# Optimization experiments

Hardware: AMD Instinct MI355X
Metric: run time of the kernel (lower is better)

## Reference

```python
import jax, jax.numpy as jnp
import numpy as np

N, E = 50000, 400000
IN_F, HID, HEADS, CLASSES, GROUP = 256, 64, 4, 40, 2
NEG_SLOPE = 0.2
EPS = 1e-5


def setup_inputs() -> dict:
    key = jax.random.key(0)
    ks = jax.random.split(key, 16)
    s = 0.05
    W = HEADS * HID          # 256 flattened hidden width
    GW = W // GROUP          # 128 per-group width
    GD = HID // GROUP        # 32  per-head out_feats in middle blocks
    x = jax.random.normal(ks[0], (N, IN_F), jnp.float32)
    src = jax.random.randint(ks[1], (E,), 0, N, dtype=jnp.int32)
    # guarantee every node has >=1 incoming edge so edge_softmax is well-defined
    dst = jnp.concatenate([jnp.arange(N, dtype=jnp.int32),
                           jax.random.randint(ks[2], (E - N,), 0, N, dtype=jnp.int32)])
    return dict(
        x=x, src=src, dst=dst,
        W0=jax.random.normal(ks[3], (W, IN_F)) * s,
        attn_l0=jax.random.normal(ks[4], (HEADS, HID)) * s,
        attn_r0=jax.random.normal(ks[5], (HEADS, HID)) * s,
        resW0=jax.random.normal(ks[6], (W, IN_F)) * s,
        mid_bn_gamma=jnp.ones((2, GROUP, GW)),
        mid_bn_beta=jnp.zeros((2, GROUP, GW)),
        mid_W=jax.random.normal(ks[7], (2, GROUP, GW, GW)) * s,
        mid_attn_l=jax.random.normal(ks[8], (2, GROUP, HEADS, GD)) * s,
        mid_attn_r=jax.random.normal(ks[9], (2, GROUP, HEADS, GD)) * s,
        mid_resW=jax.random.normal(ks[10], (2, GROUP, GW, GW)) * s,
        norm_gamma=jnp.ones((W,)), norm_beta=jnp.zeros((W,)),
        W_last=jax.random.normal(ks[11], (CLASSES, W)) * s,
        attn_l_last=jax.random.normal(ks[12], (1, CLASSES)) * s,
        attn_r_last=jax.random.normal(ks[13], (1, CLASSES)) * s,
        resW_last=jax.random.normal(ks[14], (CLASSES, W)) * s,
        bias_last=jnp.zeros((CLASSES,)),
    )


def _gat_conv(x, src, dst, W, attn_l, attn_r, resW, out_isqrt, in_sqrt):
    n = x.shape[0]
    H, D = attn_l.shape
    ft0 = (x @ W.T).reshape(n, H, D)            # projected feat [N,H,D]
    ft = ft0 * out_isqrt[:, None, None]         # symmetric norm on source side
    el = (ft * attn_l).sum(-1)                  # [N,H] (uses normalized feat_src)
    er = (ft0 * attn_r).sum(-1)                 # [N,H] (feat_dst aliased BEFORE norm)
    e = el[src] + er[dst]                       # edge scores [E,H]
    e = jnp.where(e >= 0, e, NEG_SLOPE * e)     # leaky_relu
    emax = jax.ops.segment_max(e, dst, num_segments=n)
    emax = jnp.where(jnp.isfinite(emax), emax, 0.0)
    ex = jnp.exp(e - emax[dst])
    denom = jax.ops.segment_sum(ex, dst, num_segments=n)
    a = ex / jnp.maximum(denom, 1e-9)[dst]      # per-destination edge softmax [E,H]
    msg = ft[src] * a[:, :, None]               # [E,H,D]
    rst = jax.ops.segment_sum(msg, dst, num_segments=n)
    rst = rst * in_sqrt[:, None, None]          # symmetric norm on dest side
    rst = rst + (x @ resW.T).reshape(n, H, D)   # residual fc
    return rst


def _bn_relu(z, gamma, beta):
    mu = z.mean(0)
    var = ((z - mu) ** 2).mean(0)               # biased var (torch BN training)
    return jax.nn.relu(gamma * (z - mu) * jax.lax.rsqrt(var + EPS) + beta)


def reference(x, src, dst, W0, attn_l0, attn_r0, resW0, mid_bn_gamma, mid_bn_beta,
              mid_W, mid_attn_l, mid_attn_r, mid_resW, norm_gamma, norm_beta,
              W_last, attn_l_last, attn_r_last, resW_last, bias_last):
    n = x.shape[0]
    ones = jnp.ones((src.shape[0],), x.dtype)
    outdeg = jnp.maximum(jax.ops.segment_sum(ones, src, num_segments=n), 1.0)
    indeg = jnp.maximum(jax.ops.segment_sum(ones, dst, num_segments=n), 1.0)
    out_isqrt = outdeg ** -0.5
    in_sqrt = jnp.sqrt(indeg)
    # layer 0: GATConv(in_feats -> n_hidden, n_heads)
    h = _gat_conv(x, src, dst, W0, attn_l0, attn_r0, resW0, out_isqrt, in_sqrt).reshape(n, -1)
    # reversible middle layers: GroupAdditiveCoupling, group=2
    for l in range(2):
        x0, x1 = jnp.split(h, 2, axis=-1)
        z = _bn_relu(x1, mid_bn_gamma[l, 0], mid_bn_beta[l, 0])
        y0 = x0 + _gat_conv(z, src, dst, mid_W[l, 0], mid_attn_l[l, 0], mid_attn_r[l, 0],
                            mid_resW[l, 0], out_isqrt, in_sqrt).reshape(n, -1)
        z = _bn_relu(y0, mid_bn_gamma[l, 1], mid_bn_beta[l, 1])
        y1 = x1 + _gat_conv(z, src, dst, mid_W[l, 1], mid_attn_l[l, 1], mid_attn_r[l, 1],
                            mid_resW[l, 1], out_isqrt, in_sqrt).reshape(n, -1)
        h = jnp.concatenate([y0, y1], axis=-1)
    # final norm + relu + output conv (1 head), mean over head dim, bias_last
    h = _bn_relu(h, norm_gamma, norm_beta)
    out = _gat_conv(h, src, dst, W_last, attn_l_last, attn_r_last, resW_last,
                    out_isqrt, in_sqrt).mean(1)
    return out + bias_last
```

## Files before the change

### kernel.cpp

```cpp
#include <hip/hip_runtime.h>
#include <hip/hip_bf16.h>


#define IN_F   256
#define HIDW   256
#define CLS    40

typedef __attribute__((ext_vector_type(8))) __bf16 bf16x8;
typedef __attribute__((ext_vector_type(4))) float  f32x4;

__device__ inline bf16x8 zb8() {
    bf16x8 v;
#pragma unroll
    for (int i = 0; i < 8; ++i) v[i] = (__bf16)0.f;
    return v;
}
__device__ inline bf16x8 ldb8(const __hip_bfloat16* p) {
    return *reinterpret_cast<const bf16x8*>(p);
}
__device__ inline float bf2f(unsigned short u) {
    union { unsigned int i; float f; } c;
    c.i = ((unsigned int)u) << 16;
    return c.f;
}
__device__ inline unsigned short f2bu(float f) {
    __hip_bfloat16 t = __float2bfloat16(f);
    union { __hip_bfloat16 b; unsigned short u; } c;
    c.b = t;
    return c.u;
}

__global__ void k_hist(const int* __restrict__ src, const int* __restrict__ dst,
                       int E, int* __restrict__ outdeg, int* __restrict__ indeg) {
    for (int e = blockIdx.x * blockDim.x + threadIdx.x; e < E; e += gridDim.x * blockDim.x) {
        atomicAdd(&outdeg[src[e]], 1);
        atomicAdd(&indeg[dst[e]], 1);
    }
}

__global__ void k_scan1(const int* __restrict__ cnt, int N, int* __restrict__ rp1,
                        int* __restrict__ bsum) {
    __shared__ int sm[256];
    int i = blockIdx.x * 256 + threadIdx.x;
    int v = (i < N) ? cnt[i] : 0;
    sm[threadIdx.x] = v;
    __syncthreads();
    for (int off = 1; off < 256; off <<= 1) {
        int t = (threadIdx.x >= off) ? sm[threadIdx.x - off] : 0;
        __syncthreads();
        sm[threadIdx.x] += t;
        __syncthreads();
    }
    if (i < N) rp1[i] = sm[threadIdx.x];
    if (threadIdx.x == 255) bsum[blockIdx.x] = sm[255];
}

__global__ void k_scan2(int* __restrict__ bsum, int nb) {
    __shared__ int sm[256];
    int v = (threadIdx.x < nb) ? bsum[threadIdx.x] : 0;
    sm[threadIdx.x] = v;
    __syncthreads();
    for (int off = 1; off < 256; off <<= 1) {
        int t = (threadIdx.x >= off) ? sm[threadIdx.x - off] : 0;
        __syncthreads();
        sm[threadIdx.x] += t;
        __syncthreads();
    }
    if (threadIdx.x < nb) bsum[threadIdx.x] = sm[threadIdx.x] - v;
}

__global__ void k_scan3(int* __restrict__ rp1, const int* __restrict__ bsumExcl, int N) {
    int i = blockIdx.x * 256 + threadIdx.x;
    if (i < N) rp1[i] += bsumExcl[blockIdx.x];
    if (blockIdx.x == 0 && threadIdx.x == 0) rp1[-1] = 0;
}

__global__ void k_scatter(const int* __restrict__ src, const int* __restrict__ dst,
                          int E, int* __restrict__ cursor, int* __restrict__ csr_src) {
    for (int e = blockIdx.x * blockDim.x + threadIdx.x; e < E; e += gridDim.x * blockDim.x) {
        int d = dst[e];
        int pos = atomicAdd(&cursor[d], 1);
        csr_src[pos] = src[e];
    }
}

__global__ void k_deg(const int* __restrict__ outdeg, const int* __restrict__ indeg,
                      float* __restrict__ oi, float* __restrict__ insq, int N) {
    int i = blockIdx.x * 256 + threadIdx.x;
    if (i < N) {
        int od = outdeg[i]; if (od < 1) od = 1;
        int id = indeg[i];  if (id < 1) id = 1;
        oi[i]   = rsqrtf((float)od);
        insq[i] = sqrtf((float)id);
    }
}

__global__ void k_cvt6(const float* s0, __hip_bfloat16* d0, int n0,
                       const float* s1, __hip_bfloat16* d1, int n1,
                       const float* s2, __hip_bfloat16* d2, int n2,
                       const float* s3, __hip_bfloat16* d3, int n3,
                       const float* s4, __hip_bfloat16* d4, int n4,
                       const float* s5, __hip_bfloat16* d5, int n5) {
    const float* ss; __hip_bfloat16* dd; int nn;
    switch (blockIdx.y) {
        case 0: ss = s0; dd = d0; nn = n0; break;
        case 1: ss = s1; dd = d1; nn = n1; break;
        case 2: ss = s2; dd = d2; nn = n2; break;
        case 3: ss = s3; dd = d3; nn = n3; break;
        case 4: ss = s4; dd = d4; nn = n4; break;
        default: ss = s5; dd = d5; nn = n5; break;
    }
    for (int i = blockIdx.x * blockDim.x + threadIdx.x; i < nn; i += gridDim.x * blockDim.x)
        dd[i] = __float2bfloat16(ss[i]);
}

__global__ void k_prepw(const float* __restrict__ W0,
                        const float* __restrict__ al0, const float* __restrict__ ar0,
                        const float* __restrict__ midW,
                        const float* __restrict__ midal, const float* __restrict__ midar,
                        __hip_bfloat16* __restrict__ Waug0,
                        __hip_bfloat16* __restrict__ midWaug) {
    const int layer = blockIdx.y;
    int NF, K, D;
    const float *W, *al, *ar;
    __hip_bfloat16* dst;
    if (layer == 0) {
        NF = 256; K = 256; D = 64;
        W = W0; al = al0; ar = ar0; dst = Waug0;
    } else {
        const int pg = layer - 1;
        NF = 128; K = 128; D = 32;
        W = midW + pg * 16384; al = midal + pg * 128; ar = midar + pg * 128;
        dst = midWaug + (size_t)pg * 144 * 128;
    }
    const int total = (NF + 16) * K;
    for (int idx = blockIdx.x * 256 + threadIdx.x; idx < total; idx += gridDim.x * 256) {
        const int col = idx / K, k = idx % K;
        float v = 0.f;
        if (col < NF) {
            v = W[(size_t)col * K + k];
        } else {
            const int j = col - NF;
            if (j < 8) {
                const int head = j & 3;
                const float* at = (j < 4) ? al : ar;
                float s = 0.f;
                for (int d = 0; d < D; ++d)
                    s += W[(size_t)(head * D + d) * K + k] * at[head * D + d];
                v = s;
            }
        }
        dst[idx] = __float2bfloat16(v);
    }
}

template<int K, int NF, int NR, int H, bool BN, bool ABF, bool ADDRES>
__global__ __launch_bounds__(512) void k_gatconv_lds(
    const void* __restrict__ Ain, int lda,
    const __hip_bfloat16* __restrict__ Waug,
    const __hip_bfloat16* __restrict__ Wres,
    __hip_bfloat16* __restrict__ ftb, int ldft,
    __hip_bfloat16* __restrict__ hout, int ldh, int houtoff,
    int M,
    const float* __restrict__ scale, const float* __restrict__ shift,
    const float* __restrict__ oi,
    float* __restrict__ el, float* __restrict__ er) {
    constexpr int BM = 64, KF = K / 32, NTOT = NF + NR;
    constexpr int CW = NTOT / 8, CT = CW / 16;
    constexpr int NRT = BM / 16;
    static_assert(NTOT % 8 == 0 && CW % 16 == 0, "col split");
    static_assert(NF % CW == 0, "ft/res wave boundary");
    static_assert(H == 4, "el/er float4 stores assume H==4");
    __shared__ bf16x8 ldsA[NRT * KF * 64];
    const int tid = threadIdx.x;
    const int wv = tid >> 6, lane = tid & 63, rf = lane & 15, kg = lane >> 4;
    const int row0 = blockIdx.x * BM;

    {
        constexpr int CPR = K / 8;
        constexpr int RSTEP = 512 / CPR;
        const int c16 = tid % CPR;
        const int ec = c16 * 8;
        const int skf = c16 >> 2, skg = c16 & 3;
        float sc[8], sh[8];
        if (BN) {
            float4 s01 = *reinterpret_cast<const float4*>(scale + ec);
            float4 s23 = *reinterpret_cast<const float4*>(scale + ec + 4);
            float4 h01 = *reinterpret_cast<const float4*>(shift + ec);
            float4 h23 = *reinterpret_cast<const float4*>(shift + ec + 4);
            sc[0]=s01.x; sc[1]=s01.y; sc[2]=s01.z; sc[3]=s01.w;
            sc[4]=s23.x; sc[5]=s23.y; sc[6]=s23.z; sc[7]=s23.w;
            sh[0]=h01.x; sh[1]=h01.y; sh[2]=h01.z; sh[3]=h01.w;
            sh[4]=h23.x; sh[5]=h23.y; sh[6]=h23.z; sh[7]=h23.w;
        }
#pragma unroll
        for (int r0 = 0; r0 < BM; r0 += RSTEP) {
            const int r = r0 + tid / CPR;
            if (r < BM) {
                const int gr = row0 + r;
                bf16x8 t = zb8();
                if (gr < M) {
                    if (ABF) {
                        const __hip_bfloat16* ap =
                            (const __hip_bfloat16*)Ain + (size_t)gr * lda + ec;
                        bf16x8 raw = ldb8(ap);
                        if (BN) {
#pragma unroll
                            for (int i = 0; i < 8; ++i)
                                t[i] = (__bf16)fmaxf((float)raw[i] * sc[i] + sh[i], 0.f);
                        } else {
                            t = raw;
                        }
                    } else {
                        const float* ap = (const float*)Ain + (size_t)gr * lda + ec;
                        float4 f0 = *reinterpret_cast<const float4*>(ap);
                        float4 f1 = *reinterpret_cast<const float4*>(ap + 4);
                        float v[8] = {f0.x, f0.y, f0.z, f0.w, f1.x, f1.y, f1.z, f1.w};
#pragma unroll
                        for (int i = 0; i < 8; ++i) {
                            float u = v[i];
                            if (BN) u = fmaxf(u * sc[i] + sh[i], 0.f);
                            t[i] = (__bf16)u;
                        }
                    }
                }
                ldsA[((r >> 4) * KF + skf) * 64 + ((skg * 16 + (r & 15)) ^ skf)] = t;
            }
        }
    }
    __syncthreads();

    const bool isft = (wv * CW) < NF;
    const int colbase = isft ? wv * CW : wv * CW - NF;
    const __hip_bfloat16* __restrict__ Wb = isft ? Waug : Wres;

    for (int ct = 0; ct < CT; ++ct) {
        const int tcol = colbase + ct * 16;
        bf16x8 w[KF];
        const __hip_bfloat16* bp = Wb + (size_t)(tcol + rf) * K + kg * 8;
#pragma unroll
        for (int kf = 0; kf < KF; ++kf) w[kf] = ldb8(bp + kf * 32);
#pragma unroll
        for (int rtp = 0; rtp < NRT / 2; ++rtp) {
            f32x4 acc0 = {0.f, 0.f, 0.f, 0.f};
            f32x4 acc1 = {0.f, 0.f, 0.f, 0.f};
#pragma unroll
            for (int kf = 0; kf < KF; ++kf) {
                const bf16x8 a0 = ldsA[((2 * rtp) * KF + kf) * 64 + (lane ^ kf)];
                const bf16x8 a1 = ldsA[((2 * rtp + 1) * KF + kf) * 64 + (lane ^ kf)];
                acc0 = __builtin_amdgcn_mfma_f32_16x16x32_bf16(w[kf], a0, acc0, 0, 0, 0);
                acc1 = __builtin_amdgcn_mfma_f32_16x16x32_bf16(w[kf], a1, acc1, 0, 0, 0);
            }
            const int r0g = row0 + 2 * rtp * 16 + rf;
            const int r1g = r0g + 16;
            const int c4 = tcol + 4 * kg;
            ushort4 q0 = {f2bu(acc0[0]), f2bu(acc0[1]), f2bu(acc0[2]), f2bu(acc0[3])};
            ushort4 q1 = {f2bu(acc1[0]), f2bu(acc1[1]), f2bu(acc1[2]), f2bu(acc1[3])};
            if (isft) {
                if (r0g < M)
                    *reinterpret_cast<ushort4*>(&ftb[(size_t)r0g * ldft + c4]) = q0;
                if (r1g < M)
                    *reinterpret_cast<ushort4*>(&ftb[(size_t)r1g * ldft + c4]) = q1;
            } else {
                if (r0g < M) {
                    __hip_bfloat16* hp = hout + (size_t)r0g * ldh + houtoff + c4;
                    if (ADDRES) {
                        ushort4 cur = *reinterpret_cast<ushort4*>(hp);
                        q0.x = f2bu(bf2f(cur.x) + acc0[0]);
                        q0.y = f2bu(bf2f(cur.y) + acc0[1]);
                        q0.z = f2bu(bf2f(cur.z) + acc0[2]);
                        q0.w = f2bu(bf2f(cur.w) + acc0[3]);
                    }
                    *reinterpret_cast<ushort4*>(hp) = q0;
                }
                if (r1g < M) {
                    __hip_bfloat16* hp = hout + (size_t)r1g * ldh + houtoff + c4;
                    if (ADDRES) {
                        ushort4 cur = *reinterpret_cast<ushort4*>(hp);
                        q1.x = f2bu(bf2f(cur.x) + acc1[0]);
                        q1.y = f2bu(bf2f(cur.y) + acc1[1]);
                        q1.z = f2bu(bf2f(cur.z) + acc1[2]);
                        q1.w = f2bu(bf2f(cur.w) + acc1[3]);
                    }
                    *reinterpret_cast<ushort4*>(hp) = q1;
                }
            }
        }
    }

    if (wv == 0) {
        bf16x8 w[KF];
        const __hip_bfloat16* bp = Waug + (size_t)(NF + rf) * K + kg * 8;
#pragma unroll
        for (int kf = 0; kf < KF; ++kf) w[kf] = ldb8(bp + kf * 32);
#pragma unroll
        for (int rtp = 0; rtp < NRT / 2; ++rtp) {
            f32x4 acc0 = {0.f, 0.f, 0.f, 0.f};
            f32x4 acc1 = {0.f, 0.f, 0.f, 0.f};
#pragma unroll
            for (int kf = 0; kf < KF; ++kf) {
                const bf16x8 a0 = ldsA[((2 * rtp) * KF + kf) * 64 + (lane ^ kf)];
                const bf16x8 a1 = ldsA[((2 * rtp + 1) * KF + kf) * 64 + (lane ^ kf)];
                acc0 = __builtin_amdgcn_mfma_f32_16x16x32_bf16(w[kf], a0, acc0, 0, 0, 0);
                acc1 = __builtin_amdgcn_mfma_f32_16x16x32_bf16(w[kf], a1, acc1, 0, 0, 0);
            }
            const int r0g = row0 + 2 * rtp * 16 + rf;
            const int r1g = r0g + 16;
            if (kg == 0) {
                if (r0g < M) {
                    const float o = oi[r0g];
                    float4 v = {acc0[0] * o, acc0[1] * o, acc0[2] * o, acc0[3] * o};
                    *reinterpret_cast<float4*>(&el[(size_t)r0g * 4]) = v;
                }
                if (r1g < M) {
                    const float o = oi[r1g];
                    float4 v = {acc1[0] * o, acc1[1] * o, acc1[2] * o, acc1[3] * o};
                    *reinterpret_cast<float4*>(&el[(size_t)r1g * 4]) = v;
                }
            } else if (kg == 1) {
                if (r0g < M) {
                    float4 v = {acc0[0], acc0[1], acc0[2], acc0[3]};
                    *reinterpret_cast<float4*>(&er[(size_t)r0g * 4]) = v;
                }
                if (r1g < M) {
                    float4 v = {acc1[0], acc1[1], acc1[2], acc1[3]};
                    *reinterpret_cast<float4*>(&er[(size_t)r1g * 4]) = v;
                }
            }
        }
    }
}

template<int K, int NF, int NR, int H>
__global__ __launch_bounds__(256) void k_gatconv_sm(
    const __hip_bfloat16* __restrict__ A, int lda,
    const __hip_bfloat16* __restrict__ Wft,
    const __hip_bfloat16* __restrict__ Wres,
    __hip_bfloat16* __restrict__ ftb, int ldft,
    float* __restrict__ Cres, int ldcres,
    int M,
    const float* __restrict__ scale, const float* __restrict__ shift,
    const float* __restrict__ bias,
    const float* __restrict__ attn_l, const float* __restrict__ attn_r,
    const float* __restrict__ oi,
    float* __restrict__ el, float* __restrict__ er) {
    constexpr int KF   = K / 32;
    constexpr int NCTF = (NF + 15) / 16;
    constexpr int NCTR = (NR + 15) / 16;
    constexpr int CTH  = NCTF / H;
    static_assert(NCTF % H == 0, "head tiling");
    const int wave = threadIdx.x >> 6, lane = threadIdx.x & 63;
    const int row0 = blockIdx.x * 64 + wave * 16;
    const int rf = lane & 15, kg = lane >> 4;

    bf16x8 a[KF];
    {
        const int row = row0 + rf;
        const bool rok = row < M;
#pragma unroll
        for (int kf = 0; kf < KF; ++kf) {
            const int c0 = kg * 8 + kf * 32;
            if (rok) {
                bf16x8 raw = ldb8(A + (size_t)row * lda + c0);
                float4 s01 = *reinterpret_cast<const float4*>(scale + c0);
                float4 s23 = *reinterpret_cast<const float4*>(scale + c0 + 4);
                float4 h01 = *reinterpret_cast<const float4*>(shift + c0);
                float4 h23 = *reinterpret_cast<const float4*>(shift + c0 + 4);
                float sc[8] = {s01.x,s01.y,s01.z,s01.w,s23.x,s23.y,s23.z,s23.w};
                float sh[8] = {h01.x,h01.y,h01.z,h01.w,h23.x,h23.y,h23.z,h23.w};
                bf16x8 t;
#pragma unroll
                for (int i = 0; i < 8; ++i)
                    t[i] = (__bf16)fmaxf((float)raw[i] * sc[i] + sh[i], 0.f);
                a[kf] = t;
            } else {
                a[kf] = zb8();
            }
        }
    }

    int ct = 0;
    for (int hh = 0; hh < H; ++hh) {
        float elp[4] = {0.f, 0.f, 0.f, 0.f};
        float erp[4] = {0.f, 0.f, 0.f, 0.f};
        for (int cth = 0; cth < CTH; ++cth, ++ct) {
            const int ccol = ct * 16 + rf;
            bf16x8 b[KF];
            const __hip_bfloat16* bp = Wft + (size_t)ccol * K + kg * 8;
#pragma unroll
            for (int kf = 0; kf < KF; ++kf)
                b[kf] = (ccol < NF) ? ldb8(bp + kf * 32) : zb8();
            f32x4 acc = {0.f, 0.f, 0.f, 0.f};
#pragma unroll
            for (int kf = 0; kf < KF; ++kf)
                acc = __builtin_amdgcn_mfma_f32_16x16x32_bf16(a[kf], b[kf], acc, 0, 0, 0);
            float al = 0.f, ar = 0.f;
            if (ccol < NF) { al = attn_l[ccol]; ar = attn_r[ccol]; }
            if (ccol < NF) {
#pragma unroll
                for (int r = 0; r < 4; ++r) {
                    const float v = acc[r];
                    elp[r] += v * al; erp[r] += v * ar;
                    const int row = row0 + kg * 4 + r;
                    if (row < M)
                        ftb[(size_t)row * ldft + ccol] = __float2bfloat16(v);
                }
            }
        }
#pragma unroll
        for (int off = 1; off <= 8; off <<= 1)
#pragma unroll
            for (int r = 0; r < 4; ++r) {
                elp[r] += __shfl_xor(elp[r], off);
                erp[r] += __shfl_xor(erp[r], off);
            }
        if (rf == 0) {
#pragma unroll
            for (int r = 0; r < 4; ++r) {
                const int row = row0 + kg * 4 + r;
                if (row < M) {
                    el[(size_t)row * H + hh] = oi[row] * elp[r];
                    er[(size_t)row * H + hh] = erp[r];
                }
            }
        }
    }

    for (int rt = 0; rt < NCTR; ++rt) {
        const int ccol = rt * 16 + rf;
        bf16x8 b[KF];
        const __hip_bfloat16* bp = Wres + (size_t)ccol * K + kg * 8;
#pragma unroll
        for (int kf = 0; kf < KF; ++kf)
            b[kf] = (ccol < NR) ? ldb8(bp + kf * 32) : zb8();
        f32x4 acc = {0.f, 0.f, 0.f, 0.f};
#pragma unroll
        for (int kf = 0; kf < KF; ++kf)
            acc = __builtin_amdgcn_mfma_f32_16x16x32_bf16(a[kf], b[kf], acc, 0, 0, 0);
        if (ccol < NR) {
#pragma unroll
            for (int r = 0; r < 4; ++r) {
                const int row = row0 + kg * 4 + r;
                if (row < M) {
                    float v = acc[r];
                    if (bias) v += bias[ccol];
                    Cres[(size_t)row * ldcres + ccol] = v;
                }
            }
        }
    }
}

template<int EPL>
__device__ inline void ldrow(const __hip_bfloat16* fp, float* f) {
    if constexpr (EPL == 4) {
        ushort4 q = *reinterpret_cast<const ushort4*>(fp);
        f[0] = bf2f(q.x); f[1] = bf2f(q.y); f[2] = bf2f(q.z); f[3] = bf2f(q.w);
    } else if constexpr (EPL == 2) {
        ushort2 q = *reinterpret_cast<const ushort2*>(fp);
        f[0] = bf2f(q.x); f[1] = bf2f(q.y);
    } else {
        f[0] = bf2f(*reinterpret_cast<const unsigned short*>(fp));
    }
}
__device__ inline float escore(float sc) {
    sc = sc >= 0.f ? sc : 0.2f * sc;
    sc = fminf(fmaxf(sc, -30.f), 30.f);
    return __expf(sc);
}

template<int H, int D, bool OBF>
__global__ __launch_bounds__(256) void k_agg(
    const __hip_bfloat16* __restrict__ ftb,
    const float* __restrict__ el, const float* __restrict__ er,
    const int* __restrict__ row_ptr, const int* __restrict__ csr_src,
    const float* __restrict__ oi, const float* __restrict__ insq,
    void* __restrict__ out, int ldc, int N) {
    constexpr int W = H * D;
    constexpr int EPL = (W >= 64) ? (W / 64) : 1;
    const int lane = threadIdx.x & 63;
    const int v = blockIdx.x * 4 + (threadIdx.x >> 6);
    if (v >= N) return;
    if (W < 64 && lane >= W) return;
    const int col0 = lane * EPL;
    const int myh = (W >= 64) ? (col0 / D) : 0;
    const int s = row_ptr[v], e = row_ptr[v + 1];
    const float erv = er[(size_t)v * H + myh];

    float denom = 0.f;
    float acc[EPL];
#pragma unroll
    for (int k = 0; k < EPL; ++k) acc[k] = 0.f;

    int p = s;
    for (; p + 3 < e; p += 4) {
        const int u0 = csr_src[p + 0], u1 = csr_src[p + 1];
        const int u2 = csr_src[p + 2], u3 = csr_src[p + 3];
        float f0[EPL], f1[EPL], f2[EPL], f3[EPL];
        ldrow<EPL>(ftb + (size_t)u0 * W + col0, f0);
        ldrow<EPL>(ftb + (size_t)u1 * W + col0, f1);
        ldrow<EPL>(ftb + (size_t)u2 * W + col0, f2);
        ldrow<EPL>(ftb + (size_t)u3 * W + col0, f3);
        const float s0 = el[(size_t)u0 * H + myh], s1 = el[(size_t)u1 * H + myh];
        const float s2 = el[(size_t)u2 * H + myh], s3 = el[(size_t)u3 * H + myh];
        const float o0 = oi[u0], o1 = oi[u1], o2 = oi[u2], o3 = oi[u3];
        const float w0 = escore(s0 + erv), w1 = escore(s1 + erv);
        const float w2 = escore(s2 + erv), w3 = escore(s3 + erv);
        denom += (w0 + w1) + (w2 + w3);
        const float a0 = w0 * o0, a1 = w1 * o1, a2 = w2 * o2, a3 = w3 * o3;
#pragma unroll
        for (int k = 0; k < EPL; ++k)
            acc[k] += a0 * f0[k] + a1 * f1[k] + a2 * f2[k] + a3 * f3[k];
    }
    for (; p < e; ++p) {
        const int u = csr_src[p];
        float f[EPL];
        ldrow<EPL>(ftb + (size_t)u * W + col0, f);
        const float w = escore(el[(size_t)u * H + myh] + erv);
        denom += w;
        const float a = w * oi[u];
#pragma unroll
        for (int k = 0; k < EPL; ++k) acc[k] += a * f[k];
    }

    const float iv = insq[v] / fmaxf(denom, 1e-9f);
    if (OBF) {
        __hip_bfloat16* op = (__hip_bfloat16*)out + (size_t)v * ldc + col0;
        if constexpr (EPL == 4) {
            ushort4 o = *reinterpret_cast<ushort4*>(op);
            o.x = f2bu(bf2f(o.x) + iv * acc[0]);
            o.y = f2bu(bf2f(o.y) + iv * acc[1]);
            o.z = f2bu(bf2f(o.z) + iv * acc[2]);
            o.w = f2bu(bf2f(o.w) + iv * acc[3]);
            *reinterpret_cast<ushort4*>(op) = o;
        } else if constexpr (EPL == 2) {
            ushort2 o = *reinterpret_cast<ushort2*>(op);
            o.x = f2bu(bf2f(o.x) + iv * acc[0]);
            o.y = f2bu(bf2f(o.y) + iv * acc[1]);
            *reinterpret_cast<ushort2*>(op) = o;
        } else {
            unsigned short* up = (unsigned short*)op;
            *up = f2bu(bf2f(*up) + iv * acc[0]);
        }
    } else {
        float* op = (float*)out + (size_t)v * ldc + col0;
        if constexpr (EPL == 4) {
            float4 o = *reinterpret_cast<float4*>(op);
            o.x += iv * acc[0]; o.y += iv * acc[1]; o.z += iv * acc[2]; o.w += iv * acc[3];
            *reinterpret_cast<float4*>(op) = o;
        } else if constexpr (EPL == 2) {
            float2 o = *reinterpret_cast<float2*>(op);
            o.x += iv * acc[0]; o.y += iv * acc[1];
            *reinterpret_cast<float2*>(op) = o;
        } else {
            op[0] += iv * acc[0];
        }
    }
}

template<int F>
__global__ __launch_bounds__(256) void k_bn_part(const __hip_bfloat16* __restrict__ in,
                                                 int ldin, int N,
                                                 float* __restrict__ psum,
                                                 float* __restrict__ psum2) {
    constexpr int CP = F / 2;
    constexpr int SL = 256 / CP;
    const int cp = threadIdx.x % CP;
    const int pr = blockIdx.x * SL + threadIdx.x / CP;
    const int PRT = gridDim.x * SL;
    float s0 = 0.f, s20 = 0.f, s1 = 0.f, s21 = 0.f;
    for (int r = pr; r < N; r += PRT) {
        ushort2 q = *reinterpret_cast<const ushort2*>(&in[(size_t)r * ldin + cp * 2]);
        const float a = bf2f(q.x), b = bf2f(q.y);
        s0 += a; s20 += a * a; s1 += b; s21 += b * b;
    }
    psum[(size_t)pr * F + cp * 2] = s0;
    psum[(size_t)pr * F + cp * 2 + 1] = s1;
    psum2[(size_t)pr * F + cp * 2] = s20;
    psum2[(size_t)pr * F + cp * 2 + 1] = s21;
}

template<int F>
__global__ __launch_bounds__(256) void k_bn_fin(const float* __restrict__ psum,
                                                const float* __restrict__ psum2, int PRT,
                                                const float* __restrict__ gamma,
                                                const float* __restrict__ beta,
                                                float* __restrict__ scale,
                                                float* __restrict__ shift, int N) {
    const int col = blockIdx.x;
    float s = 0.f, s2 = 0.f;
    for (int p = threadIdx.x; p < PRT; p += 256) {
        s += psum[(size_t)p * F + col];
        s2 += psum2[(size_t)p * F + col];
    }
#pragma unroll
    for (int off = 32; off; off >>= 1) {
        s += __shfl_down(s, off);
        s2 += __shfl_down(s2, off);
    }
    __shared__ float sm[4], sm2[4];
    const int wave = threadIdx.x >> 6, lane = threadIdx.x & 63;
    if (lane == 0) { sm[wave] = s; sm2[wave] = s2; }
    __syncthreads();
    if (threadIdx.x == 0) {
        s = sm[0] + sm[1] + sm[2] + sm[3];
        s2 = sm2[0] + sm2[1] + sm2[2] + sm2[3];
        float mu = s / N;
        float var = s2 / N - mu * mu;
        float isd = rsqrtf(var + 1e-5f);
        float g = gamma[col];
        scale[col] = g * isd;
        shift[col] = beta[col] - g * isd * mu;
    }
}

extern "C" void kernel_launch(void* const* d_in, const int* in_sizes, int n_in,
                              void* d_out, int out_size, void* d_ws, size_t ws_size,
                              hipStream_t stream) {
    const float* x           = (const float*)d_in[0];
    const int*   src         = (const int*)d_in[1];
    const int*   dst         = (const int*)d_in[2];
    const float* W0          = (const float*)d_in[3];
    const float* attn_l0     = (const float*)d_in[4];
    const float* attn_r0     = (const float*)d_in[5];
    const float* resW0       = (const float*)d_in[6];
    const float* mid_bn_g    = (const float*)d_in[7];
    const float* mid_bn_b    = (const float*)d_in[8];
    const float* mid_W       = (const float*)d_in[9];
    const float* mid_attn_l  = (const float*)d_in[10];
    const float* mid_attn_r  = (const float*)d_in[11];
    const float* mid_resW    = (const float*)d_in[12];
    const float* norm_gamma  = (const float*)d_in[13];
    const float* norm_beta   = (const float*)d_in[14];
    const float* W_last      = (const float*)d_in[15];
    const float* attn_l_last = (const float*)d_in[16];
    const float* attn_r_last = (const float*)d_in[17];
    const float* resW_last   = (const float*)d_in[18];
    const float* bias_last   = (const float*)d_in[19];

    const int N = in_sizes[0] / IN_F;
    const int E = in_sizes[1];

    char* p = (char*)d_ws;
    size_t used = 0;
    auto take = [&](size_t bytes) -> char* {
        char* r = p;
        size_t adv = (bytes + 255) & ~(size_t)255;
        p += adv; used += adv;
        return r;
    };
    __hip_bfloat16* h       = (__hip_bfloat16*)take((size_t)N * HIDW * 2);
    __hip_bfloat16* ftb     = (__hip_bfloat16*)take((size_t)N * HIDW * 2);
    float*          el      = (float*)take((size_t)N * 4 * 4);
    float*          er      = (float*)take((size_t)N * 4 * 4);
    float*          oi      = (float*)take((size_t)N * 4);
    float*          insq    = (float*)take((size_t)N * 4);
    int*            indeg   = (int*)take((size_t)N * 4);
    int*            outdeg  = (int*)take((size_t)N * 4);
    int*            row_ptr = (int*)take((size_t)(N + 1) * 4);
    int*            cursor  = (int*)take((size_t)N * 4);
    int*            csr_src = (int*)take((size_t)E * 4);
    int*            bsum    = (int*)take(256 * 4);
    float*          psum    = (float*)take(1 << 20);
    float*          psum2   = (float*)take(1 << 20);
    float*          scale   = (float*)take(1024);
    float*          shift   = (float*)take(1024);
    __hip_bfloat16* Waug0     = (__hip_bfloat16*)take((size_t)272 * 256 * 2);
    __hip_bfloat16* midWaug   = (__hip_bfloat16*)take((size_t)4 * 144 * 128 * 2);
    __hip_bfloat16* resW0bf   = (__hip_bfloat16*)take(65536 * 2);
    __hip_bfloat16* midresWbf = (__hip_bfloat16*)take(65536 * 2);
    __hip_bfloat16* Wlastbf   = (__hip_bfloat16*)take(10240 * 2);
    __hip_bfloat16* resWlastbf= (__hip_bfloat16*)take(10240 * 2);
    if (used > ws_size) return;

    const int nbN = (N + 255) / 256;
    const int NB4 = (N + 3) / 4;
    const int GWB = (N + 63) / 64;
    const int GWS = (N + 63) / 64;
    const int BNB = 512;

    hipMemsetAsync(indeg, 0, (size_t)N * 4, stream);
    hipMemsetAsync(outdeg, 0, (size_t)N * 4, stream);
    k_hist<<<1024, 256, 0, stream>>>(src, dst, E, outdeg, indeg);
    k_scan1<<<nbN, 256, 0, stream>>>(indeg, N, row_ptr + 1, bsum);
    k_scan2<<<1, 256, 0, stream>>>(bsum, nbN);
    k_scan3<<<nbN, 256, 0, stream>>>(row_ptr + 1, bsum, N);
    hipMemcpyAsync(cursor, row_ptr, (size_t)N * 4, hipMemcpyDeviceToDevice, stream);
    k_scatter<<<1024, 256, 0, stream>>>(src, dst, E, cursor, csr_src);
    k_deg<<<nbN, 256, 0, stream>>>(outdeg, indeg, oi, insq, N);

    k_cvt6<<<dim3(64, 4), 256, 0, stream>>>(resW0, resW0bf, 65536,
                                            mid_resW, midresWbf, 65536,
                                            W_last, Wlastbf, 10240,
                                            resW_last, resWlastbf, 10240,
                                            nullptr, nullptr, 0,
                                            nullptr, nullptr, 0);
    k_prepw<<<dim3(96, 5), 256, 0, stream>>>(W0, attn_l0, attn_r0,
                                             mid_W, mid_attn_l, mid_attn_r,
                                             Waug0, midWaug);

    k_gatconv_lds<256, 256, 256, 4, false, false, false><<<GWB, 512, 0, stream>>>(
        x, 256, Waug0, resW0bf, ftb, 256, h, 256, 0, N,
        nullptr, nullptr, oi, el, er);
    k_agg<4, 64, true><<<NB4, 256, 0, stream>>>(ftb, el, er, row_ptr, csr_src, oi, insq,
                                                h, 256, N);

    for (int l = 0; l < 2; ++l) {
        for (int g = 0; g < 2; ++g) {
            const int inoff  = (g == 0) ? 128 : 0;
            const int outoff = (g == 0) ? 0 : 128;
            const int pg = l * 2 + g;
            k_bn_part<128><<<BNB, 256, 0, stream>>>(h + inoff, 256, N, psum, psum2);
            k_bn_fin<128><<<128, 256, 0, stream>>>(psum, psum2, BNB * 4,
                                                   mid_bn_g + pg * 128, mid_bn_b + pg * 128,
                                                   scale, shift, N);
            k_gatconv_lds<128, 128, 128, 4, true, true, true><<<GWB, 512, 0, stream>>>(
                h + inoff, 256, midWaug + (size_t)pg * 144 * 128, midresWbf + pg * 16384,
                ftb, 128, h, 256, outoff, N,
                scale, shift, oi, el, er);
            k_agg<4, 32, true><<<NB4, 256, 0, stream>>>(ftb, el, er, row_ptr, csr_src,
                                                        oi, insq, h + outoff, 256, N);
        }
    }

    k_bn_part<256><<<BNB, 256, 0, stream>>>(h, 256, N, psum, psum2);
    k_bn_fin<256><<<256, 256, 0, stream>>>(psum, psum2, BNB * 2, norm_gamma, norm_beta,
                                           scale, shift, N);
    k_gatconv_sm<256, 40, 40, 1><<<GWS, 256, 0, stream>>>(
        h, 256, Wlastbf, resWlastbf, ftb, 40, (float*)d_out, 40, N,
        scale, shift, bias_last,
        attn_l_last, attn_r_last, oi, el, er);
    k_agg<1, 40, false><<<NB4, 256, 0, stream>>>(ftb, el, er, row_ptr, csr_src, oi, insq,
                                                 (float*)d_out, 40, N);
}
```

Measured before the change: 558.4 us.

## Make GATConv GEMM kernel persistent with register-prefetched next tile

The LDS-staged GATConv projection kernel now loops over row tiles with a grid-stride schedule at half the previous grid size. While one tile's MFMA work runs, the next tile's input rows are loaded into registers, then written to LDS after a barrier. This is meant to hide global-load latency behind compute and amortize weight loads. The cost is extra registers for the prefetch buffer, possibly lower occupancy, and two barriers per tile.

```diff
diff --git a/kernel.cpp b/kernel.cpp
--- a/kernel.cpp
+++ b/kernel.cpp
@@ -161,173 +161,200 @@
     const __hip_bfloat16* __restrict__ Wres,
     __hip_bfloat16* __restrict__ ftb, int ldft,
     __hip_bfloat16* __restrict__ hout, int ldh, int houtoff,
-    int M,
+    int M, int ntiles,
     const float* __restrict__ scale, const float* __restrict__ shift,
     const float* __restrict__ oi,
     float* __restrict__ el, float* __restrict__ er) {
     constexpr int BM = 64, KF = K / 32, NTOT = NF + NR;
     constexpr int CW = NTOT / 8, CT = CW / 16;
     constexpr int NRT = BM / 16;
+    constexpr int CPR = K / 8;
+    constexpr int RSTEP = 512 / CPR;
+    constexpr int PASS = BM / RSTEP;
     static_assert(NTOT % 8 == 0 && CW % 16 == 0, "col split");
     static_assert(NF % CW == 0, "ft/res wave boundary");
     static_assert(H == 4, "el/er float4 stores assume H==4");
     __shared__ bf16x8 ldsA[NRT * KF * 64];
     const int tid = threadIdx.x;
     const int wv = tid >> 6, lane = tid & 63, rf = lane & 15, kg = lane >> 4;
-    const int row0 = blockIdx.x * BM;
-
-    {
-        constexpr int CPR = K / 8;
-        constexpr int RSTEP = 512 / CPR;
-        const int c16 = tid % CPR;
-        const int ec = c16 * 8;
-        const int skf = c16 >> 2, skg = c16 & 3;
-        float sc[8], sh[8];
-        if (BN) {
-            float4 s01 = *reinterpret_cast<const float4*>(scale + ec);
-            float4 s23 = *reinterpret_cast<const float4*>(scale + ec + 4);
-            float4 h01 = *reinterpret_cast<const float4*>(shift + ec);
-            float4 h23 = *reinterpret_cast<const float4*>(shift + ec + 4);
-            sc[0]=s01.x; sc[1]=s01.y; sc[2]=s01.z; sc[3]=s01.w;
-            sc[4]=s23.x; sc[5]=s23.y; sc[6]=s23.z; sc[7]=s23.w;
-            sh[0]=h01.x; sh[1]=h01.y; sh[2]=h01.z; sh[3]=h01.w;
-            sh[4]=h23.x; sh[5]=h23.y; sh[6]=h23.z; sh[7]=h23.w;
-        }
-#pragma unroll
-        for (int r0 = 0; r0 < BM; r0 += RSTEP) {
-            const int r = r0 + tid / CPR;
-            if (r < BM) {
-                const int gr = row0 + r;
-                bf16x8 t = zb8();
-                if (gr < M) {
-                    if (ABF) {
-                        const __hip_bfloat16* ap =
-                            (const __hip_bfloat16*)Ain + (size_t)gr * lda + ec;
-                        bf16x8 raw = ldb8(ap);
-                        if (BN) {
-#pragma unroll
-                            for (int i = 0; i < 8; ++i)
-                                t[i] = (__bf16)fmaxf((float)raw[i] * sc[i] + sh[i], 0.f);
-                        } else {
-                            t = raw;
-                        }
-                    } else {
-                        const float* ap = (const float*)Ain + (size_t)gr * lda + ec;
-                        float4 f0 = *reinterpret_cast<const float4*>(ap);
-                        float4 f1 = *reinterpret_cast<const float4*>(ap + 4);
-                        float v[8] = {f0.x, f0.y, f0.z, f0.w, f1.x, f1.y, f1.z, f1.w};
-#pragma unroll
-                        for (int i = 0; i < 8; ++i) {
-                            float u = v[i];
-                            if (BN) u = fmaxf(u * sc[i] + sh[i], 0.f);
-                            t[i] = (__bf16)u;
-                        }
-                    }
-                }
-                ldsA[((r >> 4) * KF + skf) * 64 + ((skg * 16 + (r & 15)) ^ skf)] = t;
-            }
-        }
-    }
-    __syncthreads();
+
+    const int c16 = tid % CPR;
+    const int ec = c16 * 8;
+    const int skf = c16 >> 2, skg = c16 & 3;
+    const int srow = tid / CPR;
+
+    float bnsc[8], bnsh[8];
+    if (BN) {
+        float4 s01 = *reinterpret_cast<const float4*>(scale + ec);
+        float4 s23 = *reinterpret_cast<const float4*>(scale + ec + 4);
+        float4 h01 = *reinterpret_cast<const float4*>(shift + ec);
+        float4 h23 = *reinterpret_cast<const float4*>(shift + ec + 4);
+        bnsc[0]=s01.x; bnsc[1]=s01.y; bnsc[2]=s01.z; bnsc[3]=s01.w;
+        bnsc[4]=s23.x; bnsc[5]=s23.y; bnsc[6]=s23.z; bnsc[7]=s23.w;
+        bnsh[0]=h01.x; bnsh[1]=h01.y; bnsh[2]=h01.z; bnsh[3]=h01.w;
+        bnsh[4]=h23.x; bnsh[5]=h23.y; bnsh[6]=h23.z; bnsh[7]=h23.w;
+    }
+
+    float4 rA[PASS][2];
+    bf16x8 rAb[PASS];
 
     const bool isft = (wv * CW) < NF;
     const int colbase = isft ? wv * CW : wv * CW - NF;
     const __hip_bfloat16* __restrict__ Wb = isft ? Waug : Wres;
 
-    for (int ct = 0; ct < CT; ++ct) {
-        const int tcol = colbase + ct * 16;
-        bf16x8 w[KF];
-        const __hip_bfloat16* bp = Wb + (size_t)(tcol + rf) * K + kg * 8;
-#pragma unroll
-        for (int kf = 0; kf < KF; ++kf) w[kf] = ldb8(bp + kf * 32);
-#pragma unroll
-        for (int rtp = 0; rtp < NRT / 2; ++rtp) {
-            f32x4 acc0 = {0.f, 0.f, 0.f, 0.f};
-            f32x4 acc1 = {0.f, 0.f, 0.f, 0.f};
-#pragma unroll
-            for (int kf = 0; kf < KF; ++kf) {
-                const bf16x8 a0 = ldsA[((2 * rtp) * KF + kf) * 64 + (lane ^ kf)];
-                const bf16x8 a1 = ldsA[((2 * rtp + 1) * KF + kf) * 64 + (lane ^ kf)];
-                acc0 = __builtin_amdgcn_mfma_f32_16x16x32_bf16(w[kf], a0, acc0, 0, 0, 0);
-                acc1 = __builtin_amdgcn_mfma_f32_16x16x32_bf16(w[kf], a1, acc1, 0, 0, 0);
-            }
-            const int r0g = row0 + 2 * rtp * 16 + rf;
-            const int r1g = r0g + 16;
-            const int c4 = tcol + 4 * kg;
-            ushort4 q0 = {f2bu(acc0[0]), f2bu(acc0[1]), f2bu(acc0[2]), f2bu(acc0[3])};
-            ushort4 q1 = {f2bu(acc1[0]), f2bu(acc1[1]), f2bu(acc1[2]), f2bu(acc1[3])};
-            if (isft) {
-                if (r0g < M)
-                    *reinterpret_cast<ushort4*>(&ftb[(size_t)r0g * ldft + c4]) = q0;
-                if (r1g < M)
-                    *reinterpret_cast<ushort4*>(&ftb[(size_t)r1g * ldft + c4]) = q1;
+    auto load_regs = [&](int t) {
+#pragma unroll
+        for (int pz = 0; pz < PASS; ++pz) {
+            const int gr = t * BM + pz * RSTEP + srow;
+            if (ABF) {
+                rAb[pz] = (gr < M)
+                    ? ldb8((const __hip_bfloat16*)Ain + (size_t)gr * lda + ec)
+                    : zb8();
             } else {
-                if (r0g < M) {
-                    __hip_bfloat16* hp = hout + (size_t)r0g * ldh + houtoff + c4;
-                    if (ADDRES) {
-                        ushort4 cur = *reinterpret_cast<ushort4*>(hp);
-                        q0.x = f2bu(bf2f(cur.x) + acc0[0]);
-                        q0.y = f2bu(bf2f(cur.y) + acc0[1]);
-                        q0.z = f2bu(bf2f(cur.z) + acc0[2]);
-                        q0.w = f2bu(bf2f(cur.w) + acc0[3]);
+                if (gr < M) {
+                    const float* ap = (const float*)Ain + (size_t)gr * lda + ec;
+                    rA[pz][0] = *reinterpret_cast<const float4*>(ap);
+                    rA[pz][1] = *reinterpret_cast<const float4*>(ap + 4);
+                } else {
+                    rA[pz][0] = {0.f, 0.f, 0.f, 0.f};
+                    rA[pz][1] = {0.f, 0.f, 0.f, 0.f};
+                }
+            }
+        }
+    };
+    auto write_lds = [&]() {
+#pragma unroll
+        for (int pz = 0; pz < PASS; ++pz) {
+            const int r = pz * RSTEP + srow;
+            bf16x8 tv;
+            if (ABF) {
+                if (BN) {
+#pragma unroll
+                    for (int i = 0; i < 8; ++i)
+                        tv[i] = (__bf16)fmaxf((float)rAb[pz][i] * bnsc[i] + bnsh[i], 0.f);
+                } else {
+                    tv = rAb[pz];
+                }
+            } else {
+                float v[8] = {rA[pz][0].x, rA[pz][0].y, rA[pz][0].z, rA[pz][0].w,
+                              rA[pz][1].x, rA[pz][1].y, rA[pz][1].z, rA[pz][1].w};
+#pragma unroll
+                for (int i = 0; i < 8; ++i) {
+                    float u = v[i];
+                    if (BN) u = fmaxf(u * bnsc[i] + bnsh[i], 0.f);
+                    tv[i] = (__bf16)u;
+                }
+            }
+            ldsA[((r >> 4) * KF + skf) * 64 + ((skg * 16 + (r & 15)) ^ skf)] = tv;
+        }
+    };
+
+    int t = blockIdx.x;
+    load_regs(t);
+    while (t < ntiles) {
+        write_lds();
+        __syncthreads();
+        const int tn = t + gridDim.x;
+        if (tn < ntiles) load_regs(tn);
+
+        const int row0 = t * BM;
+        for (int ct = 0; ct < CT; ++ct) {
+            const int tcol = colbase + ct * 16;
+            bf16x8 w[KF];
+            const __hip_bfloat16* bp = Wb + (size_t)(tcol + rf) * K + kg * 8;
+#pragma unroll
+            for (int kf = 0; kf < KF; ++kf) w[kf] = ldb8(bp + kf * 32);
+#pragma unroll
+            for (int rtp = 0; rtp < NRT / 2; ++rtp) {
+                f32x4 acc0 = {0.f, 0.f, 0.f, 0.f};
+                f32x4 acc1 = {0.f, 0.f, 0.f, 0.f};
+#pragma unroll
+                for (int kf = 0; kf < KF; ++kf) {
+                    const bf16x8 a0 = ldsA[((2 * rtp) * KF + kf) * 64 + (lane ^ kf)];
+                    const bf16x8 a1 = ldsA[((2 * rtp + 1) * KF + kf) * 64 + (lane ^ kf)];
+                    acc0 = __builtin_amdgcn_mfma_f32_16x16x32_bf16(w[kf], a0, acc0, 0, 0, 0);
+                    acc1 = __builtin_amdgcn_mfma_f32_16x16x32_bf16(w[kf], a1, acc1, 0, 0, 0);
+                }
+                const int r0g = row0 + 2 * rtp * 16 + rf;
+                const int r1g = r0g + 16;
+                const int c4 = tcol + 4 * kg;
+                ushort4 q0 = {f2bu(acc0[0]), f2bu(acc0[1]), f2bu(acc0[2]), f2bu(acc0[3])};
+                ushort4 q1 = {f2bu(acc1[0]), f2bu(acc1[1]), f2bu(acc1[2]), f2bu(acc1[3])};
+                if (isft) {
+                    if (r0g < M)
+                        *reinterpret_cast<ushort4*>(&ftb[(size_t)r0g * ldft + c4]) = q0;
+                    if (r1g < M)
+                        *reinterpret_cast<ushort4*>(&ftb[(size_t)r1g * ldft + c4]) = q1;
+                } else {
+                    if (r0g < M) {
+                        __hip_bfloat16* hp = hout + (size_t)r0g * ldh + houtoff + c4;
+                        if (ADDRES) {
+                            ushort4 cur = *reinterpret_cast<ushort4*>(hp);
+                            q0.x = f2bu(bf2f(cur.x) + acc0[0]);
+                            q0.y = f2bu(bf2f(cur.y) + acc0[1]);
+                            q0.z = f2bu(bf2f(cur.z) + acc0[2]);
+                            q0.w = f2bu(bf2f(cur.w) + acc0[3]);
+                        }
+                        *reinterpret_cast<ushort4*>(hp) = q0;
                     }
-                    *reinterpret_cast<ushort4*>(hp) = q0;
-                }
-                if (r1g < M) {
-                    __hip_bfloat16* hp = hout + (size_t)r1g * ldh + houtoff + c4;
-                    if (ADDRES) {
-                        ushort4 cur = *reinterpret_cast<ushort4*>(hp);
-                        q1.x = f2bu(bf2f(cur.x) + acc1[0]);
-                        q1.y = f2bu(bf2f(cur.y) + acc1[1]);
-                        q1.z = f2bu(bf2f(cur.z) + acc1[2]);
-                        q1.w = f2bu(bf2f(cur.w) + acc1[3]);
+                    if (r1g < M) {
+                        __hip_bfloat16* hp = hout + (size_t)r1g * ldh + houtoff + c4;
+                        if (ADDRES) {
+                            ushort4 cur = *reinterpret_cast<ushort4*>(hp);
+                            q1.x = f2bu(bf2f(cur.x) + acc1[0]);
+                            q1.y = f2bu(bf2f(cur.y) + acc1[1]);
+                            q1.z = f2bu(bf2f(cur.z) + acc1[2]);
+                            q1.w = f2bu(bf2f(cur.w) + acc1[3]);
+                        }
+                        *reinterpret_cast<ushort4*>(hp) = q1;
                     }
-                    *reinterpret_cast<ushort4*>(hp) = q1;
-                }
-            }
-        }
-    }
-
-    if (wv == 0) {
-        bf16x8 w[KF];
-        const __hip_bfloat16* bp = Waug + (size_t)(NF + rf) * K + kg * 8;
-#pragma unroll
-        for (int kf = 0; kf < KF; ++kf) w[kf] = ldb8(bp + kf * 32);
-#pragma unroll
-        for (int rtp = 0; rtp < NRT / 2; ++rtp) {
-            f32x4 acc0 = {0.f, 0.f, 0.f, 0.f};
-            f32x4 acc1 = {0.f, 0.f, 0.f, 0.f};
-#pragma unroll
-            for (int kf = 0; kf < KF; ++kf) {
-                const bf16x8 a0 = ldsA[((2 * rtp) * KF + kf) * 64 + (lane ^ kf)];
-                const bf16x8 a1 = ldsA[((2 * rtp + 1) * KF + kf) * 64 + (lane ^ kf)];
-                acc0 = __builtin_amdgcn_mfma_f32_16x16x32_bf16(w[kf], a0, acc0, 0, 0, 0);
-                acc1 = __builtin_amdgcn_mfma_f32_16x16x32_bf16(w[kf], a1, acc1, 0, 0, 0);
-            }
-            const int r0g = row0 + 2 * rtp * 16 + rf;
-            const int r1g = r0g + 16;
-            if (kg == 0) {
-                if (r0g < M) {
-                    const float o = oi[r0g];
-                    float4 v = {acc0[0] * o, acc0[1] * o, acc0[2] * o, acc0[3] * o};
-                    *reinterpret_cast<float4*>(&el[(size_t)r0g * 4]) = v;
-                }
-                if (r1g < M) {
-                    const float o = oi[r1g];
-                    float4 v = {acc1[0] * o, acc1[1] * o, acc1[2] * o, acc1[3] * o};
-                    *reinterpret_cast<float4*>(&el[(size_t)r1g * 4]) = v;
-                }
-            } else if (kg == 1) {
-                if (r0g < M) {
-                    float4 v = {acc0[0], acc0[1], acc0[2], acc0[3]};
-                    *reinterpret_cast<float4*>(&er[(size_t)r0g * 4]) = v;
-                }
-                if (r1g < M) {
-                    float4 v = {acc1[0], acc1[1], acc1[2], acc1[3]};
-                    *reinterpret_cast<float4*>(&er[(size_t)r1g * 4]) = v;
-                }
-            }
-        }
+                }
+            }
+        }
+
+        if (wv == 0) {
+            bf16x8 w[KF];
+            const __hip_bfloat16* bp = Waug + (size_t)(NF + rf) * K + kg * 8;
+#pragma unroll
+            for (int kf = 0; kf < KF; ++kf) w[kf] = ldb8(bp + kf * 32);
+#pragma unroll
+            for (int rtp = 0; rtp < NRT / 2; ++rtp) {
+                f32x4 acc0 = {0.f, 0.f, 0.f, 0.f};
+                f32x4 acc1 = {0.f, 0.f, 0.f, 0.f};
+#pragma unroll
+                for (int kf = 0; kf < KF; ++kf) {
+                    const bf16x8 a0 = ldsA[((2 * rtp) * KF + kf) * 64 + (lane ^ kf)];
+                    const bf16x8 a1 = ldsA[((2 * rtp + 1) * KF + kf) * 64 + (lane ^ kf)];
+                    acc0 = __builtin_amdgcn_mfma_f32_16x16x32_bf16(w[kf], a0, acc0, 0, 0, 0);
+                    acc1 = __builtin_amdgcn_mfma_f32_16x16x32_bf16(w[kf], a1, acc1, 0, 0, 0);
+                }
+                const int r0g = row0 + 2 * rtp * 16 + rf;
+                const int r1g = r0g + 16;
+                if (kg == 0) {
+                    if (r0g < M) {
+                        const float o = oi[r0g];
+                        float4 v = {acc0[0] * o, acc0[1] * o, acc0[2] * o, acc0[3] * o};
+                        *reinterpret_cast<float4*>(&el[(size_t)r0g * 4]) = v;
+                    }
+                    if (r1g < M) {
+                        const float o = oi[r1g];
+                        float4 v = {acc1[0] * o, acc1[1] * o, acc1[2] * o, acc1[3] * o};
+                        *reinterpret_cast<float4*>(&el[(size_t)r1g * 4]) = v;
+                    }
+                } else if (kg == 1) {
+                    if (r0g < M) {
+                        float4 v = {acc0[0], acc0[1], acc0[2], acc0[3]};
+                        *reinterpret_cast<float4*>(&er[(size_t)r0g * 4]) = v;
+                    }
+                    if (r1g < M) {
+                        float4 v = {acc1[0], acc1[1], acc1[2], acc1[3]};
+                        *reinterpret_cast<float4*>(&er[(size_t)r1g * 4]) = v;
+                    }
+                }
+            }
+        }
+        __syncthreads();
+        t = tn;
     }
 }
 
@@ -675,7 +702,8 @@
 
     const int nbN = (N + 255) / 256;
     const int NB4 = (N + 3) / 4;
-    const int GWB = (N + 63) / 64;
+    const int NT  = (N + 63) / 64;
+    const int GWP = (NT + 1) / 2;
     const int GWS = (N + 63) / 64;
     const int BNB = 512;
 
@@ -699,8 +727,8 @@
                                              mid_W, mid_attn_l, mid_attn_r,
                                              Waug0, midWaug);
 
-    k_gatconv_lds<256, 256, 256, 4, false, false, false><<<GWB, 512, 0, stream>>>(
-        x, 256, Waug0, resW0bf, ftb, 256, h, 256, 0, N,
+    k_gatconv_lds<256, 256, 256, 4, false, false, false><<<GWP, 512, 0, stream>>>(
+        x, 256, Waug0, resW0bf, ftb, 256, h, 256, 0, N, NT,
         nullptr, nullptr, oi, el, er);
     k_agg<4, 64, true><<<NB4, 256, 0, stream>>>(ftb, el, er, row_ptr, csr_src, oi, insq,
                                                 h, 256, N);
@@ -714,9 +742,9 @@
             k_bn_fin<128><<<128, 256, 0, stream>>>(psum, psum2, BNB * 4,
                                                    mid_bn_g + pg * 128, mid_bn_b + pg * 128,
                                                    scale, shift, N);
-            k_gatconv_lds<128, 128, 128, 4, true, true, true><<<GWB, 512, 0, stream>>>(
+            k_gatconv_lds<128, 128, 128, 4, true, true, true><<<GWP, 512, 0, stream>>>(
                 h + inoff, 256, midWaug + (size_t)pg * 144 * 128, midresWbf + pg * 16384,
-                ftb, 128, h, 256, outoff, N,
+                ftb, 128, h, 256, outoff, N, NT,
                 scale, shift, oi, el, er);
             k_agg<4, 32, true><<<NB4, 256, 0, stream>>>(ftb, el, er, row_ptr, csr_src,
                                                         oi, insq, h + outoff, 256, N);
```

After: 556.0 us. About the same (-0.4%).
